# Performance work log

Measured on AMD Instinct MI355X. Metric: run time of the kernel, lower is better.

Reference implementation:

```python
import jax, jax.numpy as jnp
import numpy as np

B, N, F_IN, F_OUT, H, R = 8, 1024, 512, 512, 8, 16
HD = F_OUT // H


def fake_quant(x):
    """Simulated symmetric int8 quantize->dequantize (per-tensor)."""
    scale = jnp.maximum(jnp.max(jnp.abs(x)) / 127.0, 1e-8)
    q = jnp.clip(jnp.round(x / scale), -127.0, 127.0) * scale
    # straight-through estimator so the same fn works under vjp
    return x + jax.lax.stop_gradient(q - x)


def dora_linear(x, W, A, Bm, mag):
    """DoRA-merged linear: W' = mag * (W + B@A) / ||W + B@A||_row; y = x @ W'.T"""
    Wd = W + Bm @ A                                  # (out, in)
    col_norm = jnp.linalg.norm(Wd, axis=1, keepdims=True)  # (out, 1)
    Wp = (mag[:, None] / col_norm) * Wd
    return x @ Wp.T


def setup_inputs() -> dict:
    key = jax.random.key(0)
    ks = jax.random.split(key, 14)
    s = 0.02
    d = {
        "x": jax.random.normal(ks[0], (B, N, F_IN), jnp.float32),
        "adj_matrix": jax.random.randint(ks[1], (B, N, N), 0, 2, jnp.int32),
    }
    for i, nm in enumerate(["q", "k", "v"]):
        d[f"W_{nm}"] = jax.random.normal(ks[2 + 4 * i], (F_OUT, F_IN), jnp.float32) * s
        d[f"A_{nm}"] = jax.random.normal(ks[3 + 4 * i], (R, F_IN), jnp.float32) * s
        d[f"B_{nm}"] = jax.random.normal(ks[4 + 4 * i], (F_OUT, R), jnp.float32) * s
        d[f"m_{nm}"] = jnp.ones((F_OUT,), jnp.float32)
    return d


def reference(x, adj_matrix, W_q, A_q, B_q, m_q, W_k, A_k, B_k, m_k, W_v, A_v, B_v, m_v):
    bs, n, _ = x.shape
    # DoRA-merged Q/K/V projections -> (b, h, n, hd)
    def split_heads(t):
        return t.reshape(bs, n, H, HD).transpose(0, 2, 1, 3)
    q = split_heads(dora_linear(x, W_q, A_q, B_q, m_q))
    k = split_heads(dora_linear(x, W_k, A_k, B_k, m_k))
    v = split_heads(dora_linear(x, W_v, A_v, B_v, m_v))
    # quantized_matmul: quantize operands, dense dot-product scores (no 1/sqrt(d) in source)
    scores = jnp.einsum("bhnd,bhmd->bhnm", fake_quant(q), fake_quant(k))
    # adjacency masking: attn.masked_fill(adj == 0, -inf)
    scores = jnp.where(adj_matrix[:, None, :, :] == 0, -1e9, scores)
    # quantized_softmax + dequantize (dropout is identity in eval)
    attn = fake_quant(jax.nn.softmax(scores, axis=-1))  # (b, h, n, n)
    out = jnp.einsum("bhnm,bhmd->bhnd", attn, v)         # (b, h, n, hd)
    out = out.transpose(0, 2, 1, 3).reshape(bs, n, F_OUT)
    return out, attn
```

## Files before the change

kernel.cpp:

```cpp
#include <hip/hip_runtime.h>
#include <math.h>


typedef __attribute__((ext_vector_type(8))) short short8;
typedef __attribute__((ext_vector_type(4))) float floatx4;

#define OB_WPT   0ull
#define OB_XT    4718592ull
#define OB_QLV   OB_XT
#define OB_QRAW  36700160ull
#define OB_PS    OB_QRAW
#define OB_KRAW  53477376ull
#define OB_VT    70254592ull
#define OB_KLV   78643200ull
#define OB_RS    87031808ull
#define OB_BM    87556096ull
#define OB_AMAX  88604672ull

__device__ __forceinline__ unsigned short bf16_rne(float f) {
    unsigned int u = __float_as_uint(f);
    unsigned int r = u + 0x7fffu + ((u >> 16) & 1u);
    return (unsigned short)(r >> 16);
}
__device__ __forceinline__ float bf16_to_f(unsigned short h) {
    return __uint_as_float(((unsigned int)h) << 16);
}
__device__ __forceinline__ unsigned short bf16_exact(float f) {
    return (unsigned short)(__float_as_uint(f) >> 16);
}

__device__ __forceinline__ void dma16u(const unsigned short* g, unsigned short* l) {
    __builtin_amdgcn_global_load_lds(
        (__attribute__((address_space(1))) void*)(void*)g,
        (__attribute__((address_space(3))) void*)(void*)l, 16, 0, 0);
}

__global__ __launch_bounds__(256) void adj_bits_k(
    const int* __restrict__ adj, unsigned long long* __restrict__ bm)
{
    int tid = threadIdx.x;
    int wv = tid >> 6, lane = tid & 63;
    size_t word = (size_t)blockIdx.x * 4 + wv;
    int a = adj[word * 64 + lane];
    unsigned long long m = __ballot(a != 0);
    if (lane == 0) bm[word] = m;
}

__global__ __launch_bounds__(256) void splitx_k(
    const float* __restrict__ x, unsigned short* __restrict__ xh,
    unsigned short* __restrict__ xm, unsigned short* __restrict__ xl)
{
    int i = blockIdx.x * 256 + threadIdx.x;
    float4 v = ((const float4*)x)[i];
    ushort4 h, m, l;
    float r1, r2;
    h.x = bf16_rne(v.x); r1 = v.x - bf16_to_f(h.x);
    m.x = bf16_rne(r1);  r2 = r1 - bf16_to_f(m.x);  l.x = bf16_rne(r2);
    h.y = bf16_rne(v.y); r1 = v.y - bf16_to_f(h.y);
    m.y = bf16_rne(r1);  r2 = r1 - bf16_to_f(m.y);  l.y = bf16_rne(r2);
    h.z = bf16_rne(v.z); r1 = v.z - bf16_to_f(h.z);
    m.z = bf16_rne(r1);  r2 = r1 - bf16_to_f(m.z);  l.z = bf16_rne(r2);
    h.w = bf16_rne(v.w); r1 = v.w - bf16_to_f(h.w);
    m.w = bf16_rne(r1);  r2 = r1 - bf16_to_f(m.w);  l.w = bf16_rne(r2);
    ((ushort4*)xh)[i] = h;
    ((ushort4*)xm)[i] = m;
    ((ushort4*)xl)[i] = l;
}

__global__ __launch_bounds__(256) void build_wp3_k(
    const float* __restrict__ W_q, const float* __restrict__ A_q,
    const float* __restrict__ B_q, const float* __restrict__ m_q,
    const float* __restrict__ W_k, const float* __restrict__ A_k,
    const float* __restrict__ B_k, const float* __restrict__ m_k,
    const float* __restrict__ W_v, const float* __restrict__ A_v,
    const float* __restrict__ B_v, const float* __restrict__ m_v,
    unsigned short* __restrict__ wph, unsigned short* __restrict__ wpm,
    unsigned short* __restrict__ wpl)
{
    __shared__ float brow[16];
    __shared__ __align__(16) float wd[512];
    __shared__ float red[5];
    int o = blockIdx.x;
    int mtx = blockIdx.y;
    const float* W   = mtx == 0 ? W_q : (mtx == 1 ? W_k : W_v);
    const float* A   = mtx == 0 ? A_q : (mtx == 1 ? A_k : A_v);
    const float* Bm  = mtx == 0 ? B_q : (mtx == 1 ? B_k : B_v);
    const float* mag = mtx == 0 ? m_q : (mtx == 1 ? m_k : m_v);
    int ocol = mtx * 512 + o;
    int tid = threadIdx.x;
    if (tid < 16) brow[tid] = Bm[o * 16 + tid];
    __syncthreads();
    float ss = 0.f;
    for (int i = tid; i < 512; i += 256) {
        float acc = W[o * 512 + i];
#pragma unroll
        for (int r = 0; r < 16; ++r) acc = fmaf(brow[r], A[r * 512 + i], acc);
        wd[i] = acc;
        ss = fmaf(acc, acc, ss);
    }
#pragma unroll
    for (int off = 32; off > 0; off >>= 1) ss += __shfl_down(ss, off);
    int lane = tid & 63, wv = tid >> 6;
    if (lane == 0) red[wv] = ss;
    __syncthreads();
    if (tid == 0) red[4] = mag[o] / sqrtf(red[0] + red[1] + red[2] + red[3]);
    __syncthreads();
    float scl = red[4];
    for (int i = tid; i < 512; i += 256) {
        float v = wd[i] * scl;
        unsigned short h = bf16_rne(v);
        float r1 = v - bf16_to_f(h);
        unsigned short m = bf16_rne(r1);
        float r2 = r1 - bf16_to_f(m);
        wph[(size_t)ocol * 512 + i] = h;
        wpm[(size_t)ocol * 512 + i] = m;
        wpl[(size_t)ocol * 512 + i] = bf16_rne(r2);
    }
}

__global__ __launch_bounds__(256) void proj_mfma_k(
    const unsigned short* __restrict__ xh, const unsigned short* __restrict__ xm,
    const unsigned short* __restrict__ xl,
    const unsigned short* __restrict__ wph, const unsigned short* __restrict__ wpm,
    const unsigned short* __restrict__ wpl,
    float* __restrict__ qraw, float* __restrict__ kraw,
    unsigned short* __restrict__ vt, unsigned int* __restrict__ amax)
{
    __shared__ __align__(16) unsigned short Ah[128][32];
    __shared__ __align__(16) unsigned short Am[128][32];
    __shared__ __align__(16) unsigned short Al[128][32];
    __shared__ __align__(16) unsigned short Bh[128][32];
    __shared__ __align__(16) unsigned short Bmd[128][32];
    __shared__ __align__(16) unsigned short Bl[128][32];
    __shared__ float redmax[4];
    int tid = threadIdx.x;
    int lane = tid & 63, w = tid >> 6;
    int g = blockIdx.y * 64 + blockIdx.x;
    int xcd = g & 7, slot = g >> 3;
    int tt = (xcd << 3) | (slot / 12);
    int oo = slot - (slot / 12) * 12;
    int t0 = tt * 128;
    int o0 = oo * 128;
    int mtx = o0 >> 9;
    int wt0 = (w >> 1) * 64;
    int wo0 = (w & 1) * 64;

    floatx4 acc[4][4];
#pragma unroll
    for (int mi = 0; mi < 4; ++mi)
#pragma unroll
        for (int nj = 0; nj < 4; ++nj) acc[mi][nj] = (floatx4){0.f, 0.f, 0.f, 0.f};

    int srow = w * 32 + (lane >> 2);
    int scol = (lane & 3) * 8;
    const unsigned short* gAh = xh  + (size_t)(t0 + srow) * 512 + scol;
    const unsigned short* gAm = xm  + (size_t)(t0 + srow) * 512 + scol;
    const unsigned short* gAl = xl  + (size_t)(t0 + srow) * 512 + scol;
    const unsigned short* gBh = wph + (size_t)(o0 + srow) * 512 + scol;
    const unsigned short* gBm = wpm + (size_t)(o0 + srow) * 512 + scol;
    const unsigned short* gBl = wpl + (size_t)(o0 + srow) * 512 + scol;

    int fr = lane & 15;
    int fk = (lane >> 4) * 8;

    for (int kt = 0; kt < 16; ++kt) {
        size_t ko = (size_t)kt * 32;
        dma16u(gAh + ko,            &Ah[w * 32][0]);
        dma16u(gAh + ko + 16 * 512, &Ah[w * 32 + 16][0]);
        dma16u(gAm + ko,            &Am[w * 32][0]);
        dma16u(gAm + ko + 16 * 512, &Am[w * 32 + 16][0]);
        dma16u(gAl + ko,            &Al[w * 32][0]);
        dma16u(gAl + ko + 16 * 512, &Al[w * 32 + 16][0]);
        dma16u(gBh + ko,            &Bh[w * 32][0]);
        dma16u(gBh + ko + 16 * 512, &Bh[w * 32 + 16][0]);
        dma16u(gBm + ko,            &Bmd[w * 32][0]);
        dma16u(gBm + ko + 16 * 512, &Bmd[w * 32 + 16][0]);
        dma16u(gBl + ko,            &Bl[w * 32][0]);
        dma16u(gBl + ko + 16 * 512, &Bl[w * 32 + 16][0]);
        __syncthreads();

        short8 ah[4], am[4], al[4];
#pragma unroll
        for (int mi = 0; mi < 4; ++mi) {
            int ar = wt0 + mi * 16 + fr;
            ah[mi] = *(const short8*)&Ah[ar][fk];
            am[mi] = *(const short8*)&Am[ar][fk];
            al[mi] = *(const short8*)&Al[ar][fk];
        }
#pragma unroll
        for (int nj = 0; nj < 4; ++nj) {
            int br = wo0 + nj * 16 + fr;
            short8 bh = *(const short8*)&Bh[br][fk];
            short8 bm = *(const short8*)&Bmd[br][fk];
            short8 bl = *(const short8*)&Bl[br][fk];
#pragma unroll
            for (int mi = 0; mi < 4; ++mi) {
                acc[mi][nj] = __builtin_amdgcn_mfma_f32_16x16x32_bf16(ah[mi], bh, acc[mi][nj], 0, 0, 0);
                acc[mi][nj] = __builtin_amdgcn_mfma_f32_16x16x32_bf16(ah[mi], bm, acc[mi][nj], 0, 0, 0);
                acc[mi][nj] = __builtin_amdgcn_mfma_f32_16x16x32_bf16(am[mi], bh, acc[mi][nj], 0, 0, 0);
                acc[mi][nj] = __builtin_amdgcn_mfma_f32_16x16x32_bf16(ah[mi], bl, acc[mi][nj], 0, 0, 0);
                acc[mi][nj] = __builtin_amdgcn_mfma_f32_16x16x32_bf16(al[mi], bh, acc[mi][nj], 0, 0, 0);
                acc[mi][nj] = __builtin_amdgcn_mfma_f32_16x16x32_bf16(am[mi], bm, acc[mi][nj], 0, 0, 0);
            }
        }
        __syncthreads();
    }

    if (mtx < 2) {
        float* dst = mtx == 0 ? qraw : kraw;
        float mx = 0.f;
#pragma unroll
        for (int mi = 0; mi < 4; ++mi) {
#pragma unroll
            for (int r = 0; r < 4; ++r) {
                int t = t0 + wt0 + mi * 16 + (lane >> 4) * 4 + r;
                int b = t >> 10, n = t & 1023;
#pragma unroll
                for (int nj = 0; nj < 4; ++nj) {
                    int o = o0 + wo0 + nj * 16 + fr;
                    int h = (o >> 6) & 7, d = o & 63;
                    float val = acc[mi][nj][r];
                    dst[((size_t)(b * 8 + h) * 1024 + n) * 64 + d] = val;
                    mx = fmaxf(mx, fabsf(val));
                }
            }
        }
#pragma unroll
        for (int off = 32; off > 0; off >>= 1) mx = fmaxf(mx, __shfl_down(mx, off));
        if ((tid & 63) == 0) redmax[tid >> 6] = mx;
        __syncthreads();
        if (tid == 0) {
            float m2 = fmaxf(fmaxf(redmax[0], redmax[1]), fmaxf(redmax[2], redmax[3]));
            atomicMax(&amax[mtx], __float_as_uint(m2));
        }
    } else {
#pragma unroll
        for (int mi = 0; mi < 4; ++mi) {
            int t0r = t0 + wt0 + mi * 16 + (lane >> 4) * 4;
            int b = t0r >> 10, n0 = t0r & 1023;
            int ml = n0 & 63, mb = n0 - ml;
#pragma unroll
            for (int nj = 0; nj < 4; ++nj) {
                int o = o0 + wo0 + nj * 16 + fr;
                int h = (o >> 6) & 7, d = o & 63;
                int mlp = (ml & 7) | ((((ml >> 3) ^ d) & 7) << 3);
                ushort4 hv;
                hv.x = bf16_rne(acc[mi][nj][0]);
                hv.y = bf16_rne(acc[mi][nj][1]);
                hv.z = bf16_rne(acc[mi][nj][2]);
                hv.w = bf16_rne(acc[mi][nj][3]);
                *(ushort4*)(vt + ((size_t)((b * 8 + h) * 64 + d)) * 1024 + mb + mlp) = hv;
            }
        }
    }
}

__global__ __launch_bounds__(256) void quant2_k(
    const float* __restrict__ qraw, const float* __restrict__ kraw,
    const unsigned int* __restrict__ amax,
    unsigned short* __restrict__ qlv, unsigned short* __restrict__ klv)
{
    int m = blockIdx.y;
    const float* raw = m ? kraw : qraw;
    unsigned short* lv = m ? klv : qlv;
    float scale = fmaxf(__uint_as_float(amax[m]) / 127.f, 1e-8f);
    int i = blockIdx.x * 256 + threadIdx.x;
    float4 v = ((const float4*)raw)[i];
    float l0 = fminf(fmaxf(rintf(v.x / scale), -127.f), 127.f);
    float l1 = fminf(fmaxf(rintf(v.y / scale), -127.f), 127.f);
    float l2 = fminf(fmaxf(rintf(v.z / scale), -127.f), 127.f);
    float l3 = fminf(fmaxf(rintf(v.w / scale), -127.f), 127.f);
    ushort4 o;
    o.x = bf16_exact(l0); o.y = bf16_exact(l1);
    o.z = bf16_exact(l2); o.w = bf16_exact(l3);
    int idx4 = i;
    if (m) {
        int elem0 = i * 4;
        int d0 = elem0 & 63;
        int n = (elem0 >> 6) & 1023;
        int dp = (d0 & 7) | ((((d0 >> 3) ^ n) & 7) << 3);
        idx4 = (elem0 - d0 + dp) >> 2;
    }
    ((ushort4*)lv)[idx4] = o;
}

__global__ __launch_bounds__(256) void attn_stats_k(
    const unsigned short* __restrict__ qlv, const unsigned short* __restrict__ klv,
    const unsigned long long* __restrict__ bm, const unsigned int* __restrict__ amax,
    float2* __restrict__ psums)
{
    __shared__ __align__(16) unsigned short Ks[2][64][64];
    int tid = threadIdx.x;
    int lane = tid & 63, w = tid >> 6;
    int m_ = lane & 15, quad = lane >> 4;
    int g = blockIdx.z * 1024 + blockIdx.y * 16 + blockIdx.x;
    int xcd = g & 7, slot = g >> 3;
    int bh = (xcd << 3) | (slot >> 6);
    int rem = slot & 63;
    int qt = rem >> 2, qtr = rem & 3;
    int b = bh >> 3;
    int rowbase = qt * 64 + w * 16;
    float sq = fmaxf(__uint_as_float(amax[0]) / 127.f, 1e-8f);
    float sk = fmaxf(__uint_as_float(amax[1]) / 127.f, 1e-8f);
    float ss = sq * sk;

    const unsigned short* qp = qlv + ((size_t)bh * 1024 + rowbase + m_) * 64;
    short8 Aq0 = *(const short8*)(qp + quad * 8);
    short8 Aq1 = *(const short8*)(qp + 32 + quad * 8);
    const unsigned long long* bmb = bm + ((size_t)b * 1024 + rowbase) * 16;

    const unsigned short* gK = klv + ((size_t)bh * 1024 + w * 16) * 64 + lane * 8;
    int sw0 = ((quad ^ m_) & 7) << 3;
    int sw1 = (((4 + quad) ^ m_) & 7) << 3;

    float mrun[4], lrun[4];
#pragma unroll
    for (int r = 0; r < 4; ++r) { mrun[r] = -1e9f; lrun[r] = 0.f; }

    {
        size_t off = (size_t)(qtr * 4) * 4096;
        dma16u(gK + off,       &Ks[0][w * 16][0]);
        dma16u(gK + off + 512, &Ks[0][w * 16 + 8][0]);
    }
    __asm__ volatile("s_waitcnt vmcnt(0)" ::: "memory");
    __builtin_amdgcn_s_barrier();

    for (int ci = 0; ci < 4; ++ci) {
        int c = qtr * 4 + ci;
        int buf = ci & 1;
        if (ci < 3) {
            size_t off = (size_t)(c + 1) * 4096;
            dma16u(gK + off,       &Ks[buf ^ 1][w * 16][0]);
            dma16u(gK + off + 512, &Ks[buf ^ 1][w * 16 + 8][0]);
        }
        unsigned long long mk[4];
#pragma unroll
        for (int r = 0; r < 4; ++r) mk[r] = bmb[(quad * 4 + r) * 16 + c];
        float sv[4][4];
#pragma unroll
        for (int s = 0; s < 4; ++s) {
            short8 B0 = *(const short8*)&Ks[buf][s * 16 + m_][sw0];
            short8 B1 = *(const short8*)&Ks[buf][s * 16 + m_][sw1];
            floatx4 Cv = {0.f, 0.f, 0.f, 0.f};
            Cv = __builtin_amdgcn_mfma_f32_16x16x32_bf16(Aq0, B0, Cv, 0, 0, 0);
            Cv = __builtin_amdgcn_mfma_f32_16x16x32_bf16(Aq1, B1, Cv, 0, 0, 0);
            int colbit = s * 16 + m_;
#pragma unroll
            for (int r = 0; r < 4; ++r)
                sv[r][s] = ((mk[r] >> colbit) & 1ull) ? Cv[r] * ss : -1e9f;
        }
#pragma unroll
        for (int r = 0; r < 4; ++r) {
            float tm = fmaxf(fmaxf(sv[r][0], sv[r][1]), fmaxf(sv[r][2], sv[r][3]));
            float mn = fmaxf(mrun[r], tm);
            float e = __expf(sv[r][0] - mn) + __expf(sv[r][1] - mn)
                    + __expf(sv[r][2] - mn) + __expf(sv[r][3] - mn);
            lrun[r] = fmaf(lrun[r], __expf(mrun[r] - mn), e);
            mrun[r] = mn;
        }
        __asm__ volatile("s_waitcnt vmcnt(0)" ::: "memory");
        __builtin_amdgcn_s_barrier();
    }

#pragma unroll
    for (int r = 0; r < 4; ++r) {
        float m = mrun[r], l = lrun[r];
#pragma unroll
        for (int off = 1; off < 16; off <<= 1) {
            float mo = __shfl_xor(m, off);
            float lo = __shfl_xor(l, off);
            float mn = fmaxf(m, mo);
            l = l * __expf(m - mn) + lo * __expf(mo - mn);
            m = mn;
        }
        if (m_ == 0)
            psums[(size_t)qtr * 65536 + (size_t)bh * 1024 + rowbase + quad * 4 + r] =
                make_float2(m, l);
    }
}

__global__ __launch_bounds__(256) void stats_merge_k(
    const float2* __restrict__ ps, float2* __restrict__ rowstats,
    unsigned int* __restrict__ amax_attn)
{
    int row = blockIdx.x * 256 + threadIdx.x;
    float2 a = ps[row];
    float m = a.x, l = a.y;
#pragma unroll
    for (int q = 1; q < 4; ++q) {
        float2 bq = ps[(size_t)q * 65536 + row];
        float mn = fmaxf(m, bq.x);
        l = l * __expf(m - mn) + bq.y * __expf(bq.x - mn);
        m = mn;
    }
    rowstats[row] = make_float2(m, l);
    float inv = 1.0f / l;
#pragma unroll
    for (int off = 1; off < 64; off <<= 1) inv = fmaxf(inv, __shfl_xor(inv, off));
    if ((threadIdx.x & 63) == 0) atomicMax(amax_attn, __float_as_uint(inv));
}

__global__ __launch_bounds__(256) void attn_out_k(
    const unsigned short* __restrict__ qlv, const unsigned short* __restrict__ klv,
    const unsigned short* __restrict__ vt,
    const unsigned long long* __restrict__ bm, const unsigned int* __restrict__ amax,
    const float2* __restrict__ rowstats,
    float* __restrict__ attn, float* __restrict__ out)
{
    __shared__ __align__(16) unsigned short Ks[2][64][64];
    __shared__ __align__(16) unsigned short Vs[2][64][64];
    __shared__ unsigned short pl[4][2][16][68];
    int tid = threadIdx.x;
    int lane = tid & 63, w = tid >> 6;
    int m_ = lane & 15, quad = lane >> 4;
    int g = blockIdx.y * 16 + blockIdx.x;
    int xcd = g & 7, slot = g >> 3;
    int bh = (xcd << 3) | (slot >> 4);
    int qt = slot & 15;
    int b = bh >> 3, h = bh & 7;
    int rowbase = qt * 64 + w * 16;
    float sq = fmaxf(__uint_as_float(amax[0]) / 127.f, 1e-8f);
    float sk = fmaxf(__uint_as_float(amax[1]) / 127.f, 1e-8f);
    float ss = sq * sk;
    float sa = fmaxf(__uint_as_float(amax[2]) / 127.f, 1e-8f);
    float inv_sa = 1.0f / sa;

    const unsigned short* qp = qlv + ((size_t)bh * 1024 + rowbase + m_) * 64;
    short8 Aq0 = *(const short8*)(qp + quad * 8);
    short8 Aq1 = *(const short8*)(qp + 32 + quad * 8);
    const unsigned long long* bmb = bm + ((size_t)b * 1024 + rowbase) * 16;

    const unsigned short* gK  = klv + ((size_t)bh * 1024 + w * 16) * 64 + lane * 8;
    const unsigned short* gV  = vt + ((size_t)(bh * 64 + w * 16 + (lane >> 3))) * 1024 + (lane & 7) * 8;
    const unsigned short* gV2 = gV + 8 * 1024;
    int sw0 = ((quad ^ m_) & 7) << 3;
    int sw1 = (((4 + quad) ^ m_) & 7) << 3;

    float mrow[4], rlr[4];
#pragma unroll
    for (int r = 0; r < 4; ++r) {
        float2 st = rowstats[(size_t)bh * 1024 + rowbase + quad * 4 + r];
        mrow[r] = st.x;
        rlr[r] = 1.0f / st.y;
    }
    floatx4 acc[4];
#pragma unroll
    for (int r = 0; r < 4; ++r) acc[r] = (floatx4){0.f, 0.f, 0.f, 0.f};

    float* attn_b = attn + ((size_t)bh << 20);

#define STG(bf, cc) do {                                                  \
        dma16u(gK + (size_t)(cc) * 4096,       &Ks[bf][w * 16][0]);       \
        dma16u(gK + (size_t)(cc) * 4096 + 512, &Ks[bf][w * 16 + 8][0]);   \
        dma16u(gV + (cc) * 64,                 &Vs[bf][w * 16][0]);       \
        dma16u(gV2 + (cc) * 64,                &Vs[bf][w * 16 + 8][0]);   \
    } while (0)

    STG(0, 0);
    __asm__ volatile("s_waitcnt vmcnt(0)" ::: "memory");
    __builtin_amdgcn_s_barrier();

    for (int ci = 0; ci < 16; ++ci) {
        int c = ci;
        int buf = ci & 1;
        if (ci + 1 < 16) STG(buf ^ 1, ci + 1);
        short8 Vb0[4], Vb1[4];
#pragma unroll
        for (int dt = 0; dt < 4; ++dt) {
            Vb0[dt] = *(const short8*)&Vs[buf][dt * 16 + m_][sw0];
            Vb1[dt] = *(const short8*)&Vs[buf][dt * 16 + m_][sw1];
        }
        unsigned long long mk[4];
#pragma unroll
        for (int r = 0; r < 4; ++r) mk[r] = bmb[(quad * 4 + r) * 16 + c];
        unsigned short* plw = &pl[w][ci & 1][0][0];
#pragma unroll
        for (int s = 0; s < 4; ++s) {
            short8 B0 = *(const short8*)&Ks[buf][s * 16 + m_][sw0];
            short8 B1 = *(const short8*)&Ks[buf][s * 16 + m_][sw1];
            floatx4 Cv = {0.f, 0.f, 0.f, 0.f};
            Cv = __builtin_amdgcn_mfma_f32_16x16x32_bf16(Aq0, B0, Cv, 0, 0, 0);
            Cv = __builtin_amdgcn_mfma_f32_16x16x32_bf16(Aq1, B1, Cv, 0, 0, 0);
            int colbit = s * 16 + m_;
#pragma unroll
            for (int r = 0; r < 4; ++r) {
                float sval = ((mk[r] >> colbit) & 1ull) ? Cv[r] * ss : -1e9f;
                float p = __expf(sval - mrow[r]) * rlr[r];
                float lv = fminf(rintf(p * inv_sa), 127.f);
                plw[(quad * 4 + r) * 68 + colbit] = bf16_exact(lv);
            }
        }
        __asm__ volatile("s_waitcnt lgkmcnt(0)" ::: "memory");
        short8 Ap0 = *(const short8*)&pl[w][ci & 1][m_][quad * 8];
        short8 Ap1 = *(const short8*)&pl[w][ci & 1][m_][32 + quad * 8];
#pragma unroll
        for (int dt = 0; dt < 4; ++dt) {
            acc[dt] = __builtin_amdgcn_mfma_f32_16x16x32_bf16(Ap0, Vb0[dt], acc[dt], 0, 0, 0);
            acc[dt] = __builtin_amdgcn_mfma_f32_16x16x32_bf16(Ap1, Vb1[dt], acc[dt], 0, 0, 0);
        }
#pragma unroll
        for (int it = 0; it < 4; ++it) {
            int rrow = it * 4 + quad, col = m_ * 4;
            uint2 pk = *(const uint2*)&pl[w][ci & 1][rrow][col];
            float4 av;
            av.x = bf16_to_f((unsigned short)(pk.x & 0xffff)) * sa;
            av.y = bf16_to_f((unsigned short)(pk.x >> 16)) * sa;
            av.z = bf16_to_f((unsigned short)(pk.y & 0xffff)) * sa;
            av.w = bf16_to_f((unsigned short)(pk.y >> 16)) * sa;
            *(float4*)(attn_b + (((size_t)(rowbase + rrow)) << 10) + c * 64 + col) = av;
        }
        __asm__ volatile("s_waitcnt vmcnt(0)" ::: "memory");
        __builtin_amdgcn_s_barrier();
    }
#undef STG
#pragma unroll
    for (int dt = 0; dt < 4; ++dt)
#pragma unroll
        for (int r = 0; r < 4; ++r) {
            int n = rowbase + quad * 4 + r;
            int d = dt * 16 + m_;
            out[(size_t)(b * 1024 + n) * 512 + h * 64 + d] = acc[dt][r] * sa;
        }
}

extern "C" void kernel_launch(void* const* d_in, const int* in_sizes, int n_in,
                              void* d_out, int out_size, void* d_ws, size_t ws_size,
                              hipStream_t stream)
{
    (void)in_sizes; (void)n_in; (void)out_size; (void)ws_size;
    const float* x   = (const float*)d_in[0];
    const int*   adj = (const int*)d_in[1];
    const float* W_q = (const float*)d_in[2];
    const float* A_q = (const float*)d_in[3];
    const float* B_q = (const float*)d_in[4];
    const float* m_q = (const float*)d_in[5];
    const float* W_k = (const float*)d_in[6];
    const float* A_k = (const float*)d_in[7];
    const float* B_k = (const float*)d_in[8];
    const float* m_k = (const float*)d_in[9];
    const float* W_v = (const float*)d_in[10];
    const float* A_v = (const float*)d_in[11];
    const float* B_v = (const float*)d_in[12];
    const float* m_v = (const float*)d_in[13];

    char* ws = (char*)d_ws;
    unsigned short* wph = (unsigned short*)(ws + OB_WPT);
    unsigned short* wpm = (unsigned short*)(ws + OB_WPT + 1572864);
    unsigned short* wpl = (unsigned short*)(ws + OB_WPT + 3145728);
    unsigned short* xh  = (unsigned short*)(ws + OB_XT);
    unsigned short* xm  = (unsigned short*)(ws + OB_XT + 8388608);
    unsigned short* xl  = (unsigned short*)(ws + OB_XT + 16777216);
    float* qraw         = (float*)(ws + OB_QRAW);
    float* kraw         = (float*)(ws + OB_KRAW);
    unsigned short* qlv = (unsigned short*)(ws + OB_QLV);
    unsigned short* klv = (unsigned short*)(ws + OB_KLV);
    unsigned short* vt  = (unsigned short*)(ws + OB_VT);
    float2* rowstats    = (float2*)(ws + OB_RS);
    float2* psums       = (float2*)(ws + OB_PS);
    unsigned long long* bmask = (unsigned long long*)(ws + OB_BM);
    unsigned int* amax  = (unsigned int*)(ws + OB_AMAX);

    float* out_base  = (float*)d_out;
    float* attn_base = out_base + 4194304;

    hipMemsetAsync(amax, 0, 16, stream);

    adj_bits_k<<<32768, 256, 0, stream>>>(adj, bmask);
    splitx_k<<<4096, 256, 0, stream>>>(x, xh, xm, xl);

    build_wp3_k<<<dim3(512, 3), 256, 0, stream>>>(W_q, A_q, B_q, m_q,
                                                  W_k, A_k, B_k, m_k,
                                                  W_v, A_v, B_v, m_v, wph, wpm, wpl);
    proj_mfma_k<<<dim3(64, 12), 256, 0, stream>>>(xh, xm, xl, wph, wpm, wpl,
                                                  qraw, kraw, vt, amax);
    quant2_k<<<dim3(4096, 2), 256, 0, stream>>>(qraw, kraw, amax, qlv, klv);

    attn_stats_k<<<dim3(16, 64, 4), 256, 0, stream>>>(qlv, klv, bmask, amax, psums);
    stats_merge_k<<<256, 256, 0, stream>>>(psums, rowstats, amax + 2);
    attn_out_k<<<dim3(16, 64), 256, 0, stream>>>(qlv, klv, vt, bmask, amax,
                                                 rowstats, attn_base, out_base);
}
```

Baseline: 524.8 us.

## Fuse split-K softmax stats pass with merge kernel, drop partial sums buffer

The attention stats kernel now processes all 16 key chunks per block instead of splitting them over four blocks. It keeps four per-quarter running max/sum accumulators and merges them in registers, then writes rowstats directly. The per-block max of 1/l goes through a single atomicMax, which removes the separate stats_merge kernel and its global psums round trip. In exchange the grid is four times smaller with a longer serial loop per block, reducing parallelism and latency hiding.

```diff
diff --git a/kernel.cpp b/kernel.cpp
--- a/kernel.cpp
+++ b/kernel.cpp
@@ -9,7 +9,6 @@
 #define OB_XT    4718592ull
 #define OB_QLV   OB_XT
 #define OB_QRAW  36700160ull
-#define OB_PS    OB_QRAW
 #define OB_KRAW  53477376ull
 #define OB_VT    70254592ull
 #define OB_KLV   78643200ull
@@ -287,17 +286,17 @@
 __global__ __launch_bounds__(256) void attn_stats_k(
     const unsigned short* __restrict__ qlv, const unsigned short* __restrict__ klv,
     const unsigned long long* __restrict__ bm, const unsigned int* __restrict__ amax,
-    float2* __restrict__ psums)
+    float2* __restrict__ rowstats, unsigned int* __restrict__ amax_attn)
 {
     __shared__ __align__(16) unsigned short Ks[2][64][64];
+    __shared__ float redv[4];
     int tid = threadIdx.x;
     int lane = tid & 63, w = tid >> 6;
     int m_ = lane & 15, quad = lane >> 4;
-    int g = blockIdx.z * 1024 + blockIdx.y * 16 + blockIdx.x;
+    int g = blockIdx.y * 16 + blockIdx.x;
     int xcd = g & 7, slot = g >> 3;
-    int bh = (xcd << 3) | (slot >> 6);
-    int rem = slot & 63;
-    int qt = rem >> 2, qtr = rem & 3;
+    int bh = (xcd << 3) | (slot >> 4);
+    int qt = slot & 15;
     int b = bh >> 3;
     int rowbase = qt * 64 + w * 16;
     float sq = fmaxf(__uint_as_float(amax[0]) / 127.f, 1e-8f);
@@ -313,29 +312,28 @@
     int sw0 = ((quad ^ m_) & 7) << 3;
     int sw1 = (((4 + quad) ^ m_) & 7) << 3;
 
-    float mrun[4], lrun[4];
-#pragma unroll
-    for (int r = 0; r < 4; ++r) { mrun[r] = -1e9f; lrun[r] = 0.f; }
-
-    {
-        size_t off = (size_t)(qtr * 4) * 4096;
-        dma16u(gK + off,       &Ks[0][w * 16][0]);
-        dma16u(gK + off + 512, &Ks[0][w * 16 + 8][0]);
-    }
+    float mq[4][4], lq[4][4];
+#pragma unroll
+    for (int qq = 0; qq < 4; ++qq)
+#pragma unroll
+        for (int r = 0; r < 4; ++r) { mq[qq][r] = -1e9f; lq[qq][r] = 0.f; }
+
+    dma16u(gK,       &Ks[0][w * 16][0]);
+    dma16u(gK + 512, &Ks[0][w * 16 + 8][0]);
     __asm__ volatile("s_waitcnt vmcnt(0)" ::: "memory");
     __builtin_amdgcn_s_barrier();
 
-    for (int ci = 0; ci < 4; ++ci) {
-        int c = qtr * 4 + ci;
+    for (int ci = 0; ci < 16; ++ci) {
         int buf = ci & 1;
-        if (ci < 3) {
-            size_t off = (size_t)(c + 1) * 4096;
+        if (ci + 1 < 16) {
+            size_t off = (size_t)(ci + 1) * 4096;
             dma16u(gK + off,       &Ks[buf ^ 1][w * 16][0]);
             dma16u(gK + off + 512, &Ks[buf ^ 1][w * 16 + 8][0]);
         }
+        int qq = ci >> 2;
         unsigned long long mk[4];
 #pragma unroll
-        for (int r = 0; r < 4; ++r) mk[r] = bmb[(quad * 4 + r) * 16 + c];
+        for (int r = 0; r < 4; ++r) mk[r] = bmb[(quad * 4 + r) * 16 + ci];
         float sv[4][4];
 #pragma unroll
         for (int s = 0; s < 4; ++s) {
@@ -352,52 +350,52 @@
 #pragma unroll
         for (int r = 0; r < 4; ++r) {
             float tm = fmaxf(fmaxf(sv[r][0], sv[r][1]), fmaxf(sv[r][2], sv[r][3]));
-            float mn = fmaxf(mrun[r], tm);
+            float mn = fmaxf(mq[qq][r], tm);
             float e = __expf(sv[r][0] - mn) + __expf(sv[r][1] - mn)
                     + __expf(sv[r][2] - mn) + __expf(sv[r][3] - mn);
-            lrun[r] = fmaf(lrun[r], __expf(mrun[r] - mn), e);
-            mrun[r] = mn;
+            lq[qq][r] = fmaf(lq[qq][r], __expf(mq[qq][r] - mn), e);
+            mq[qq][r] = mn;
         }
         __asm__ volatile("s_waitcnt vmcnt(0)" ::: "memory");
         __builtin_amdgcn_s_barrier();
     }
 
+    float iv = 0.f;
 #pragma unroll
     for (int r = 0; r < 4; ++r) {
-        float m = mrun[r], l = lrun[r];
-#pragma unroll
-        for (int off = 1; off < 16; off <<= 1) {
-            float mo = __shfl_xor(m, off);
-            float lo = __shfl_xor(l, off);
-            float mn = fmaxf(m, mo);
-            l = l * __expf(m - mn) + lo * __expf(mo - mn);
+        float M[4], L[4];
+#pragma unroll
+        for (int qq = 0; qq < 4; ++qq) {
+            float m = mq[qq][r], l = lq[qq][r];
+#pragma unroll
+            for (int off = 1; off < 16; off <<= 1) {
+                float mo = __shfl_xor(m, off);
+                float lo = __shfl_xor(l, off);
+                float mn = fmaxf(m, mo);
+                l = l * __expf(m - mn) + lo * __expf(mo - mn);
+                m = mn;
+            }
+            M[qq] = m; L[qq] = l;
+        }
+        float m = M[0], l = L[0];
+#pragma unroll
+        for (int qq = 1; qq < 4; ++qq) {
+            float mn = fmaxf(m, M[qq]);
+            l = l * __expf(m - mn) + L[qq] * __expf(M[qq] - mn);
             m = mn;
         }
         if (m_ == 0)
-            psums[(size_t)qtr * 65536 + (size_t)bh * 1024 + rowbase + quad * 4 + r] =
-                make_float2(m, l);
-    }
-}
-
-__global__ __launch_bounds__(256) void stats_merge_k(
-    const float2* __restrict__ ps, float2* __restrict__ rowstats,
-    unsigned int* __restrict__ amax_attn)
-{
-    int row = blockIdx.x * 256 + threadIdx.x;
-    float2 a = ps[row];
-    float m = a.x, l = a.y;
-#pragma unroll
-    for (int q = 1; q < 4; ++q) {
-        float2 bq = ps[(size_t)q * 65536 + row];
-        float mn = fmaxf(m, bq.x);
-        l = l * __expf(m - mn) + bq.y * __expf(bq.x - mn);
-        m = mn;
-    }
-    rowstats[row] = make_float2(m, l);
-    float inv = 1.0f / l;
-#pragma unroll
-    for (int off = 1; off < 64; off <<= 1) inv = fmaxf(inv, __shfl_xor(inv, off));
-    if ((threadIdx.x & 63) == 0) atomicMax(amax_attn, __float_as_uint(inv));
+            rowstats[(size_t)bh * 1024 + rowbase + quad * 4 + r] = make_float2(m, l);
+        iv = fmaxf(iv, 1.0f / l);
+    }
+#pragma unroll
+    for (int off = 1; off < 64; off <<= 1) iv = fmaxf(iv, __shfl_xor(iv, off));
+    if (lane == 0) redv[w] = iv;
+    __syncthreads();
+    if (tid == 0) {
+        float m2 = fmaxf(fmaxf(redv[0], redv[1]), fmaxf(redv[2], redv[3]));
+        atomicMax(amax_attn, __float_as_uint(m2));
+    }
 }
 
 __global__ __launch_bounds__(256) void attn_out_k(
@@ -556,7 +554,6 @@
     unsigned short* klv = (unsigned short*)(ws + OB_KLV);
     unsigned short* vt  = (unsigned short*)(ws + OB_VT);
     float2* rowstats    = (float2*)(ws + OB_RS);
-    float2* psums       = (float2*)(ws + OB_PS);
     unsigned long long* bmask = (unsigned long long*)(ws + OB_BM);
     unsigned int* amax  = (unsigned int*)(ws + OB_AMAX);
 
@@ -575,8 +572,8 @@
                                                   qraw, kraw, vt, amax);
     quant2_k<<<dim3(4096, 2), 256, 0, stream>>>(qraw, kraw, amax, qlv, klv);
 
-    attn_stats_k<<<dim3(16, 64, 4), 256, 0, stream>>>(qlv, klv, bmask, amax, psums);
-    stats_merge_k<<<256, 256, 0, stream>>>(psums, rowstats, amax + 2);
+    attn_stats_k<<<dim3(16, 64), 256, 0, stream>>>(qlv, klv, bmask, amax,
+                                                   rowstats, amax + 2);
     attn_out_k<<<dim3(16, 64), 256, 0, stream>>>(qlv, klv, vt, bmask, amax,
                                                  rowstats, attn_base, out_base);
 }
```

Result: no change. 522.8 us (-0.4%).
